# Performance work log

Measured on AMD Instinct MI355X. Metric: run time of the kernel, lower is better.

The kernel has to match this reference:

```python
import jax, jax.numpy as jnp
import numpy as np

GAMMA = 2.0
EPS = 1e-06
LAMBDA_DISTANCE = 1.0
LAMBDA_NORMAL = 0.01
LAMBDA_LAPLACIAN = 0.1
CLS = 1


def vertex_normals(v, f, eps=EPS):
    # v: [N,3], f: [F,3] int. Scatter face normals to vertices, then normalize.
    fv = v[f]  # [F,3,3]
    fn = jnp.cross(fv[:, 1] - fv[:, 0], fv[:, 2] - fv[:, 0])  # [F,3]
    vn = jnp.zeros_like(v)
    vn = vn.at[f[:, 0]].add(fn).at[f[:, 1]].add(fn).at[f[:, 2]].add(fn)
    norm = jnp.maximum(jnp.linalg.norm(vn, axis=-1, keepdims=True), eps)
    return vn / norm


def squared_cdist(a, b):
    # [Na,3] x [Nb,3] -> squared euclidean distances [Na,Nb] (clamped >= 0)
    a2 = jnp.sum(a * a, axis=1)[:, None]
    b2 = jnp.sum(b * b, axis=1)[None, :]
    d2 = a2 + b2 - 2.0 * (a @ b.T)
    return jnp.maximum(d2, 0.0)


def sample_binary_targets(label, v, cls=CLS):
    # Nearest-neighbor grid_sample, align_corners=True, padding zeros.
    # grid = 2*v - 1 -> voxel index = round(v * (size-1)); v[:,0]->W, v[:,1]->H, v[:,2]->D.
    D, H, W = label.shape[2], label.shape[3], label.shape[4]
    ix = jnp.round(v[:, 0] * (W - 1)).astype(jnp.int32)
    iy = jnp.round(v[:, 1] * (H - 1)).astype(jnp.int32)
    iz = jnp.round(v[:, 2] * (D - 1)).astype(jnp.int32)
    inb = (ix >= 0) & (ix < W) & (iy >= 0) & (iy < H) & (iz >= 0) & (iz < D)
    ixc = jnp.clip(ix, 0, W - 1)
    iyc = jnp.clip(iy, 0, H - 1)
    izc = jnp.clip(iz, 0, D - 1)
    vals = (label[0, 0, izc, iyc, ixc] == cls).astype(jnp.float32)
    return jnp.where(inb, vals, 0.0)


def spatial_consistency_loss(rel_pos, targets, gamma=GAMMA, eps=EPS):
    p = jnp.clip(rel_pos, eps, 1.0 - eps)
    pos = targets > 0.5
    pc = jnp.sum(pos).astype(p.dtype)
    tot = jnp.asarray(p.shape[0], p.dtype)
    nc = tot - pc
    alpha = nc / (tot + eps)
    lpos = -alpha * jnp.power(1.0 - p, gamma) * jnp.log(p)
    lneg = -(1.0 - alpha) * jnp.power(p, gamma) * jnp.log(1.0 - p)
    return jnp.sum(jnp.where(pos, lpos, lneg)) / (tot + eps)


def laplacian_uniform(v, f):
    # Uniform mesh Laplacian smoothing: || mean(neighbors) - v ||, averaged.
    i = jnp.concatenate([f[:, 0], f[:, 1], f[:, 2], f[:, 1], f[:, 2], f[:, 0]])
    j = jnp.concatenate([f[:, 1], f[:, 2], f[:, 0], f[:, 0], f[:, 1], f[:, 2]])
    nsum = jnp.zeros_like(v).at[i].add(v[j])
    deg = jnp.zeros((v.shape[0],), v.dtype).at[i].add(1.0)
    lap = nsum / jnp.maximum(deg, 1.0)[:, None] - v
    return jnp.mean(jnp.linalg.norm(lap, axis=1))


def loss_forward(pred_vertices, relative_positions, gt_vertices, pred_faces, gt_faces, label):
    gt_v = jax.lax.stop_gradient(gt_vertices)  # gt comes from label volume; detached in original
    gt_normals = vertex_normals(gt_v, gt_faces)
    # spatial (focal-style) loss
    targets = sample_binary_targets(label, pred_vertices)
    spatial = spatial_consistency_loss(relative_positions, targets)
    # chamfer-style squared surface distance
    d2 = squared_cdist(pred_vertices, gt_v)  # [Np,Ng]
    distance = jnp.mean(jnp.min(d2, axis=1)) + jnp.mean(jnp.min(d2, axis=0))
    # normal consistency vs nearest gt vertex
    pred_normals = vertex_normals(pred_vertices, pred_faces)
    nearest = jnp.argmin(d2, axis=1)
    normal = jnp.mean((pred_normals - gt_normals[nearest]) ** 2)
    # uniform laplacian smoothing
    laplacian = laplacian_uniform(pred_vertices, pred_faces)
    total = spatial + LAMBDA_DISTANCE * distance + LAMBDA_NORMAL * normal + LAMBDA_LAPLACIAN * laplacian
    return total


def setup_inputs() -> dict:
    key = jax.random.key(0)
    k1, k2, k3, k4, k5, k6 = jax.random.split(key, 6)
    Np, Ng = 8192, 12000
    pred_vertices = jax.random.uniform(k1, (Np, 3), dtype=jnp.float32)
    relative_positions = jax.random.uniform(k2, (Np,), dtype=jnp.float32)
    gt_vertices = jax.random.uniform(k3, (Ng, 3), dtype=jnp.float32)
    pred_faces = jax.random.randint(k4, (2 * Np, 3), 0, Np, dtype=jnp.int32)
    gt_faces = jax.random.randint(k5, (2 * Ng, 3), 0, Ng, dtype=jnp.int32)
    label = jax.random.randint(k6, (1, 1, 96, 96, 96), 0, 2, dtype=jnp.int32)
    return {"pred_vertices": pred_vertices, "relative_positions": relative_positions,
            "gt_vertices": gt_vertices, "pred_faces": pred_faces,
            "gt_faces": gt_faces, "label": label}


def reference(pred_vertices, relative_positions, gt_vertices, pred_faces, gt_faces, label):
    return loss_forward(pred_vertices, relative_positions, gt_vertices, pred_faces, gt_faces, label)
```

## Files before the change

### kernel.cpp

```cpp
#include <hip/hip_runtime.h>
#include <math.h>

#define NP 8192
#define NG 12000
#define NFP 16384
#define NFG 24000
#define EPSF 1e-6f

#define GR 16
#define NC (GR*GR*GR)
#define HCELL 0.0625f
#define QL 16

#define N_ZERO 101545
#define ZERO_BLOCKS ((N_ZERO + 1023) / 1024)
#define D1_BLOCKS (2 + ZERO_BLOCKS)

#define QPBLK 64
#define PQB (NP / QPBLK)
#define GQB ((NG + QPBLK - 1) / QPBLK)
#define FB  ((NFG + NFP + 1023) / 1024)
#define D2_BLOCKS (PQB + GQB + FB)

#define CAPP  4608
#define CWCAP 1312

#define FIN_BLOCKS (NP / 256)

static constexpr size_t OFF_STARTP = 0;
static constexpr size_t OFF_STARTG = 16640;
static constexpr size_t OFF_SORTP  = 33280;
static constexpr size_t OFF_SORTG  = 164352;
static constexpr size_t OFF_GTN    = 356352;
static constexpr size_t OFF_PNN    = 500352;
static constexpr size_t OFF_NSUM   = 598656;
static constexpr size_t OFF_DEG    = 696960;
static constexpr size_t OFF_NEAR   = 729728;
static constexpr size_t OFF_ACCUM  = 762496;
static constexpr size_t OFF_DONE   = 762528;

__device__ __forceinline__ int cell_of(float x) {
    int c = (int)(x * (float)GR);
    return min(max(c, 0), GR - 1);
}

__device__ __forceinline__ void build_cells(const float* __restrict__ pts, int n,
                                            unsigned* __restrict__ start,
                                            float4* __restrict__ sorted,
                                            unsigned* h, unsigned* wsum) {
    int t = threadIdx.x;
    int lane = t & 63, wid = t >> 6;
    for (int i = t; i < NC; i += 1024) h[i] = 0u;
    __syncthreads();
    for (int i = t; i < n; i += 1024) {
        int c = (cell_of(pts[3*i+2]) * GR + cell_of(pts[3*i+1])) * GR + cell_of(pts[3*i]);
        atomicAdd(&h[c], 1u);
    }
    __syncthreads();
    unsigned a0 = h[4*t], a1 = h[4*t+1], a2 = h[4*t+2], a3 = h[4*t+3];
    unsigned tsum = a0 + a1 + a2 + a3;
    unsigned x = tsum;
    #pragma unroll
    for (int off = 1; off < 64; off <<= 1) {
        unsigned y = __shfl_up(x, off, 64);
        if (lane >= off) x += y;
    }
    if (lane == 63) wsum[wid] = x;
    __syncthreads();
    if (t < 16) {
        unsigned w = wsum[t];
        #pragma unroll
        for (int off = 1; off < 16; off <<= 1) {
            unsigned y = __shfl_up(w, off, 64);
            if (t >= off) w += y;
        }
        wsum[t] = w;
    }
    __syncthreads();
    unsigned base = (wid ? wsum[wid-1] : 0u) + (x - tsum);
    unsigned e0 = base, e1 = base + a0, e2 = base + a0 + a1, e3 = base + a0 + a1 + a2;
    start[4*t] = e0; start[4*t+1] = e1; start[4*t+2] = e2; start[4*t+3] = e3;
    h[4*t] = e0; h[4*t+1] = e1; h[4*t+2] = e2; h[4*t+3] = e3;
    __syncthreads();
    for (int i = t; i < n; i += 1024) {
        float px = pts[3*i], py = pts[3*i+1], pz = pts[3*i+2];
        int c = (cell_of(pz) * GR + cell_of(py)) * GR + cell_of(px);
        unsigned pos = atomicAdd(&h[c], 1u);
        sorted[pos] = make_float4(px, py, pz, __int_as_float(i));
    }
    if (t == 0) start[NC] = (unsigned)n;
}

__global__ __launch_bounds__(1024) void build_kernel(const float* __restrict__ pred,
                                                     const float* __restrict__ gt,
                                                     unsigned* __restrict__ startP,
                                                     unsigned* __restrict__ startG,
                                                     float4* __restrict__ sortP,
                                                     float4* __restrict__ sortG,
                                                     float* __restrict__ zero) {
    __shared__ unsigned h[NC];
    __shared__ unsigned wsum[16];
    if (blockIdx.x == 0) {
        build_cells(pred, NP, startP, sortP, h, wsum);
    } else if (blockIdx.x == 1) {
        build_cells(gt, NG, startG, sortG, h, wsum);
    } else {
        int i = (blockIdx.x - 2) * 1024 + threadIdx.x;
        if (i < N_ZERO) zero[i] = 0.0f;
    }
}

__device__ __forceinline__ float wave_sum(float x) {
    #pragma unroll
    for (int o = 32; o > 0; o >>= 1) x += __shfl_down(x, o, 64);
    return x;
}

__device__ __forceinline__ unsigned long long u64min(unsigned long long a,
                                                     unsigned long long b) {
    return a < b ? a : b;
}

__device__ __forceinline__ unsigned long long pack_key(float px, float py, float pz,
                                                       float4 q) {
    float ddx = px - q.x, ddy = py - q.y, ddz = pz - q.z;
    float d2 = fmaf(ddx, ddx, fmaf(ddy, ddy, ddz*ddz));
    return ((unsigned long long)__float_as_uint(d2) << 32) |
           (unsigned)__float_as_int(q.w);
}

__device__ unsigned long long group_nn(int lane, float px, float py, float pz,
                                       const float4* __restrict__ Sg,
                                       const unsigned* __restrict__ CSg,
                                       const float4* Sl, const unsigned* CSl,
                                       int c_lo, unsigned p_lo, bool staged) {
    int cx = cell_of(px), cy = cell_of(py), cz = cell_of(pz);
    unsigned long long best = 0xFFFFFFFFFFFFFFFFULL;
    {
        int x0 = max(cx - 1, 0), x1 = min(cx + 1, GR - 1);
        unsigned long long lb = 0xFFFFFFFFFFFFFFFFULL;
        for (int k = lane; k < 9; k += QL) {
            int z = cz + k / 3 - 1, y = cy + k % 3 - 1;
            if (z >= 0 && z < GR && y >= 0 && y < GR) {
                int rowbase = (z * GR + y) * GR;
                if (staged) {
                    unsigned s0 = CSl[rowbase + x0 - c_lo];
                    unsigned s1 = CSl[rowbase + x1 + 1 - c_lo];
                    for (unsigned u = s0; u < s1; ++u)
                        lb = u64min(lb, pack_key(px, py, pz, Sl[u - p_lo]));
                } else {
                    unsigned s0 = CSg[rowbase + x0];
                    unsigned s1 = CSg[rowbase + x1 + 1];
                    for (unsigned u = s0; u < s1; ++u)
                        lb = u64min(lb, pack_key(px, py, pz, Sg[u]));
                }
            }
        }
        best = lb;
        #pragma unroll
        for (int m = 1; m < QL; m <<= 1)
            best = u64min(best, (unsigned long long)__shfl_xor((long long)best, m, 64));
        bool covered = (cx - 1 <= 0) & (cx + 1 >= GR - 1) &
                       (cy - 1 <= 0) & (cy + 1 >= GR - 1) &
                       (cz - 1 <= 0) & (cz + 1 >= GR - 1);
        float blo = 1.0e30f;
        if (cx - 1 > 0)      blo = fminf(blo, px - (float)(cx - 1) * HCELL);
        if (cx + 1 < GR - 1) blo = fminf(blo, (float)(cx + 2) * HCELL - px);
        if (cy - 1 > 0)      blo = fminf(blo, py - (float)(cy - 1) * HCELL);
        if (cy + 1 < GR - 1) blo = fminf(blo, (float)(cy + 2) * HCELL - py);
        if (cz - 1 > 0)      blo = fminf(blo, pz - (float)(cz - 1) * HCELL);
        if (cz + 1 < GR - 1) blo = fminf(blo, (float)(cz + 2) * HCELL - pz);
        float bd2 = __uint_as_float((unsigned)(best >> 32));
        if (covered || (bd2 <= blo * blo)) return best;
    }
    for (int r = 2; ; ++r) {
        int w = 2 * r + 1;
        int nrows = w * w;
        int x0 = max(cx - r, 0), x1 = min(cx + r, GR - 1);
        unsigned long long lb = 0xFFFFFFFFFFFFFFFFULL;
        for (int k = lane; k < nrows; k += QL) {
            int z = cz + k / w - r, y = cy + k % w - r;
            if (z >= 0 && z < GR && y >= 0 && y < GR) {
                int rowbase = (z * GR + y) * GR;
                unsigned s0 = CSg[rowbase + x0];
                unsigned s1 = CSg[rowbase + x1 + 1];
                for (unsigned u = s0; u < s1; ++u)
                    lb = u64min(lb, pack_key(px, py, pz, Sg[u]));
            }
        }
        best = u64min(best, lb);
        #pragma unroll
        for (int m = 1; m < QL; m <<= 1)
            best = u64min(best, (unsigned long long)__shfl_xor((long long)best, m, 64));
        bool covered = (cx - r <= 0) & (cx + r >= GR - 1) &
                       (cy - r <= 0) & (cy + r >= GR - 1) &
                       (cz - r <= 0) & (cz + r >= GR - 1);
        if (covered) break;
        float blo = 1.0e30f;
        if (cx - r > 0)      blo = fminf(blo, px - (float)(cx - r) * HCELL);
        if (cx + r < GR - 1) blo = fminf(blo, (float)(cx + r + 1) * HCELL - px);
        if (cy - r > 0)      blo = fminf(blo, py - (float)(cy - r) * HCELL);
        if (cy + r < GR - 1) blo = fminf(blo, (float)(cy + r + 1) * HCELL - py);
        if (cz - r > 0)      blo = fminf(blo, pz - (float)(cz - r) * HCELL);
        if (cz + r < GR - 1) blo = fminf(blo, (float)(cz + r + 1) * HCELL - pz);
        float bd2 = __uint_as_float((unsigned)(best >> 32));
        if (bd2 <= blo * blo) break;
    }
    return best;
}

__global__ __launch_bounds__(1024) void work_kernel(const float* __restrict__ pred,
                                                    const int* __restrict__ pf,
                                                    const float* __restrict__ gt,
                                                    const int* __restrict__ gf,
                                                    const float4* __restrict__ sortP,
                                                    const float4* __restrict__ sortG,
                                                    const unsigned* __restrict__ startP,
                                                    const unsigned* __restrict__ startG,
                                                    float* __restrict__ gtn,
                                                    float* __restrict__ pnn,
                                                    float* __restrict__ nsum,
                                                    float* __restrict__ deg,
                                                    int* __restrict__ nearestIdx,
                                                    float* __restrict__ accum) {
    __shared__ float4 lpts[CAPP];
    __shared__ unsigned lcs[CWCAP];
    __shared__ float qacc;
    __shared__ int s_info[4];
    int b = blockIdx.x, t = threadIdx.x;

    if (b < PQB + GQB) {
        bool is_pred = (b < PQB);
        const float4*   Q  = is_pred ? sortP  : sortG;
        const float4*   S  = is_pred ? sortG  : sortP;
        const unsigned* CS = is_pred ? startG : startP;
        int qbase = (is_pred ? b : (b - PQB)) * QPBLK;
        int nq = min(QPBLK, (is_pred ? NP : NG) - qbase);

        if (t == 0) {
            qacc = 0.0f;
            float4 qf = Q[qbase], ql = Q[qbase + nq - 1];
            int z_lo = cell_of(qf.z), z_hi = cell_of(ql.z);
            int c_lo  = max(z_lo - 1, 0) * (GR * GR);
            int c_end = min(z_hi + 2, GR) * (GR * GR);
            int cw = c_end - c_lo + 1;
            unsigned p_lo = CS[c_lo], p_hi = CS[c_end];
            int np = (int)(p_hi - p_lo);
            bool ok = (cw <= CWCAP) && (np <= CAPP);
            s_info[0] = c_lo; s_info[1] = (int)p_lo; s_info[2] = np;
            s_info[3] = ok ? cw : -cw;
        }
        __syncthreads();
        int c_lo = s_info[0];
        unsigned p_lo = (unsigned)s_info[1];
        int np = s_info[2];
        int cw = s_info[3];
        bool staged = (cw > 0);
        if (staged) {
            for (int i = t; i < np; i += 1024) lpts[i] = S[p_lo + i];
            for (int i = t; i < cw; i += 1024) lcs[i]  = CS[c_lo + i];
        }
        __syncthreads();

        int lane = t & (QL - 1), group = t >> 4;
        float r0 = 0.0f;
        if (group < nq) {
            int qid = qbase + group;
            float4 P = Q[qid];
            unsigned long long key = group_nn(lane, P.x, P.y, P.z, S, CS,
                                              lpts, lcs, c_lo, p_lo, staged);
            if (lane == 0) {
                r0 = __uint_as_float((unsigned)(key >> 32));
                if (is_pred)
                    nearestIdx[__float_as_int(P.w)] = (int)(unsigned)(key & 0xffffffffu);
            }
        }
        r0 = wave_sum(r0);
        if ((t & 63) == 0) atomicAdd(&qacc, r0);
        __syncthreads();
        if (t == 0) atomicAdd(&accum[is_pred ? 0 : 6], qacc);
    } else {
        int f = (b - PQB - GQB) * 1024 + t;
        if (f < NFG) {
            int i0 = gf[3*f], i1 = gf[3*f+1], i2 = gf[3*f+2];
            float ax = gt[3*i0], ay = gt[3*i0+1], az = gt[3*i0+2];
            float bx = gt[3*i1], by = gt[3*i1+1], bz = gt[3*i1+2];
            float cx = gt[3*i2], cy = gt[3*i2+1], cz = gt[3*i2+2];
            float ux = bx-ax, uy = by-ay, uz = bz-az;
            float wx = cx-ax, wy = cy-ay, wz = cz-az;
            float nx = uy*wz - uz*wy, ny = uz*wx - ux*wz, nz = ux*wy - uy*wx;
            atomicAdd(&gtn[3*i0+0], nx); atomicAdd(&gtn[3*i0+1], ny); atomicAdd(&gtn[3*i0+2], nz);
            atomicAdd(&gtn[3*i1+0], nx); atomicAdd(&gtn[3*i1+1], ny); atomicAdd(&gtn[3*i1+2], nz);
            atomicAdd(&gtn[3*i2+0], nx); atomicAdd(&gtn[3*i2+1], ny); atomicAdd(&gtn[3*i2+2], nz);
        } else if (f < NFG + NFP) {
            int u = f - NFG;
            int i0 = pf[3*u], i1 = pf[3*u+1], i2 = pf[3*u+2];
            float ax = pred[3*i0], ay = pred[3*i0+1], az = pred[3*i0+2];
            float bx = pred[3*i1], by = pred[3*i1+1], bz = pred[3*i1+2];
            float cx = pred[3*i2], cy = pred[3*i2+1], cz = pred[3*i2+2];
            float ux = bx-ax, uy = by-ay, uz = bz-az;
            float wx = cx-ax, wy = cy-ay, wz = cz-az;
            float nx = uy*wz - uz*wy, ny = uz*wx - ux*wz, nz = ux*wy - uy*wx;
            atomicAdd(&pnn[3*i0+0], nx); atomicAdd(&pnn[3*i0+1], ny); atomicAdd(&pnn[3*i0+2], nz);
            atomicAdd(&pnn[3*i1+0], nx); atomicAdd(&pnn[3*i1+1], ny); atomicAdd(&pnn[3*i1+2], nz);
            atomicAdd(&pnn[3*i2+0], nx); atomicAdd(&pnn[3*i2+1], ny); atomicAdd(&pnn[3*i2+2], nz);
            atomicAdd(&nsum[3*i0+0], bx+cx); atomicAdd(&nsum[3*i0+1], by+cy); atomicAdd(&nsum[3*i0+2], bz+cz);
            atomicAdd(&nsum[3*i1+0], cx+ax); atomicAdd(&nsum[3*i1+1], cy+ay); atomicAdd(&nsum[3*i1+2], cz+az);
            atomicAdd(&nsum[3*i2+0], ax+bx); atomicAdd(&nsum[3*i2+1], ay+by); atomicAdd(&nsum[3*i2+2], az+bz);
            atomicAdd(&deg[i0], 2.0f); atomicAdd(&deg[i1], 2.0f); atomicAdd(&deg[i2], 2.0f);
        }
    }
}

__global__ __launch_bounds__(256) void finish_kernel(const float* __restrict__ pred,
                                                     const float* __restrict__ relpos,
                                                     const int* __restrict__ label,
                                                     const float* __restrict__ pnn,
                                                     const float* __restrict__ gtn,
                                                     const float* __restrict__ nsum,
                                                     const float* __restrict__ deg,
                                                     const int* __restrict__ nearestIdx,
                                                     float* __restrict__ accum,
                                                     unsigned* __restrict__ done,
                                                     float* __restrict__ out) {
    int v = blockIdx.x * 256 + threadIdx.x;
    float px = pred[3*v], py = pred[3*v+1], pz = pred[3*v+2];
    int nearest = nearestIdx[v];

    float ax = pnn[3*v], ay = pnn[3*v+1], az = pnn[3*v+2];
    float an = fmaxf(sqrtf(ax*ax + ay*ay + az*az), EPSF);
    float gx = gtn[3*nearest], gy = gtn[3*nearest+1], gz = gtn[3*nearest+2];
    float gn = fmaxf(sqrtf(gx*gx + gy*gy + gz*gz), EPSF);
    float nx = ax/an - gx/gn, ny = ay/an - gy/gn, nz = az/an - gz/gn;
    float sse = nx*nx + ny*ny + nz*nz;

    float d = fmaxf(deg[v], 1.0f);
    float lx = nsum[3*v]/d - px, ly = nsum[3*v+1]/d - py, lz = nsum[3*v+2]/d - pz;
    float lapn = sqrtf(lx*lx + ly*ly + lz*lz);

    int ix = (int)rintf(px * 95.0f), iy = (int)rintf(py * 95.0f), iz = (int)rintf(pz * 95.0f);
    bool inb = (ix >= 0) & (ix < 96) & (iy >= 0) & (iy < 96) & (iz >= 0) & (iz < 96);
    int ixc = min(max(ix, 0), 95), iyc = min(max(iy, 0), 95), izc = min(max(iz, 0), 95);
    bool pos = inb && (label[(izc*96 + iyc)*96 + ixc] == 1);

    float p = fminf(fmaxf(relpos[v], EPSF), 1.0f - EPSF);
    float om = 1.0f - p;
    float pcnt = 0.0f, sx = 0.0f, sy = 0.0f;
    if (pos) { pcnt = 1.0f; sx = om*om*logf(p); }
    else     { sy = p*p*logf(om); }

    float r1 = wave_sum(sse), r2 = wave_sum(lapn), r3 = wave_sum(pcnt);
    float r4 = wave_sum(sx),  r5 = wave_sum(sy);
    __shared__ float bsum[5];
    __shared__ bool isLast;
    if (threadIdx.x < 5) bsum[threadIdx.x] = 0.0f;
    __syncthreads();
    if ((threadIdx.x & 63) == 0) {
        atomicAdd(&bsum[0], r1); atomicAdd(&bsum[1], r2); atomicAdd(&bsum[2], r3);
        atomicAdd(&bsum[3], r4); atomicAdd(&bsum[4], r5);
    }
    __syncthreads();
    if (threadIdx.x == 0) {
        atomicAdd(&accum[1], bsum[0]); atomicAdd(&accum[2], bsum[1]);
        atomicAdd(&accum[3], bsum[2]); atomicAdd(&accum[4], bsum[3]);
        atomicAdd(&accum[5], bsum[4]);
        __threadfence();
        unsigned prev = atomicAdd(done, 1u);
        isLast = (prev == FIN_BLOCKS - 1);
    }
    __syncthreads();
    if (isLast && threadIdx.x == 0) {
        __threadfence();
        float sum_row = __hip_atomic_load(&accum[0], __ATOMIC_RELAXED, __HIP_MEMORY_SCOPE_AGENT);
        float sse_t   = __hip_atomic_load(&accum[1], __ATOMIC_RELAXED, __HIP_MEMORY_SCOPE_AGENT);
        float lap_t   = __hip_atomic_load(&accum[2], __ATOMIC_RELAXED, __HIP_MEMORY_SCOPE_AGENT);
        float pc      = __hip_atomic_load(&accum[3], __ATOMIC_RELAXED, __HIP_MEMORY_SCOPE_AGENT);
        float SX      = __hip_atomic_load(&accum[4], __ATOMIC_RELAXED, __HIP_MEMORY_SCOPE_AGENT);
        float SY      = __hip_atomic_load(&accum[5], __ATOMIC_RELAXED, __HIP_MEMORY_SCOPE_AGENT);
        float sum_col = __hip_atomic_load(&accum[6], __ATOMIC_RELAXED, __HIP_MEMORY_SCOPE_AGENT);
        float tot = (float)NP;
        float alpha = (tot - pc) / (tot + EPSF);
        float spatial = (-alpha * SX - (1.0f - alpha) * SY) / (tot + EPSF);
        float distance = sum_row / (float)NP + sum_col / (float)NG;
        float normal = sse_t / (float)(NP * 3);
        float lapm = lap_t / (float)NP;
        out[0] = spatial + 1.0f * distance + 0.01f * normal + 0.1f * lapm;
    }
}

extern "C" void kernel_launch(void* const* d_in, const int* in_sizes, int n_in,
                              void* d_out, int out_size, void* d_ws, size_t ws_size,
                              hipStream_t stream) {
    const float* pred   = (const float*)d_in[0];
    const float* relpos = (const float*)d_in[1];
    const float* gt     = (const float*)d_in[2];
    const int*   pfaces = (const int*)d_in[3];
    const int*   gfaces = (const int*)d_in[4];
    const int*   label  = (const int*)d_in[5];
    float* out = (float*)d_out;

    char* ws = (char*)d_ws;
    unsigned* startP  = (unsigned*)(ws + OFF_STARTP);
    unsigned* startG  = (unsigned*)(ws + OFF_STARTG);
    float4*   sortP   = (float4*)(ws + OFF_SORTP);
    float4*   sortG   = (float4*)(ws + OFF_SORTG);
    float*    gtn     = (float*)(ws + OFF_GTN);
    float*    pnn     = (float*)(ws + OFF_PNN);
    float*    nsum    = (float*)(ws + OFF_NSUM);
    float*    deg     = (float*)(ws + OFF_DEG);
    int*      nearest = (int*)(ws + OFF_NEAR);
    float*    accum   = (float*)(ws + OFF_ACCUM);
    unsigned* done    = (unsigned*)(ws + OFF_DONE);

    hipLaunchKernelGGL(build_kernel, dim3(D1_BLOCKS), dim3(1024), 0, stream,
                       pred, gt, startP, startG, sortP, sortG,
                       (float*)(ws + OFF_GTN));
    hipLaunchKernelGGL(work_kernel, dim3(D2_BLOCKS), dim3(1024), 0, stream,
                       pred, pfaces, gt, gfaces, sortP, sortG, startP, startG,
                       gtn, pnn, nsum, deg, nearest, accum);
    hipLaunchKernelGGL(finish_kernel, dim3(FIN_BLOCKS), dim3(256), 0, stream,
                       pred, relpos, label, pnn, gtn, nsum, deg, nearest,
                       accum, done, out);
}
```

Baseline: 132.2 us.

## Move face scatter into build kernel, zero with memset, split query kernel

The face-normal and Laplacian scatter atomics move from the query kernel into the build kernel, so they run alongside the two single-block grid builds instead of competing with the NN queries. Workspace zeroing becomes a hipMemsetAsync ahead of the build kernel. The first NN ring now iterates the 27 individual neighbour cells instead of 9 x-rows. The cost is an extra memset launch, and the per-cell loop spreads the work over more lanes but adds more index lookups.

```diff
diff --git a/kernel.cpp b/kernel.cpp
--- a/kernel.cpp
+++ b/kernel.cpp
@@ -12,15 +12,13 @@
 #define HCELL 0.0625f
 #define QL 16
 
-#define N_ZERO 101545
-#define ZERO_BLOCKS ((N_ZERO + 1023) / 1024)
-#define D1_BLOCKS (2 + ZERO_BLOCKS)
+#define FB ((NFG + NFP + 1023) / 1024)
+#define D1_BLOCKS (2 + FB)
 
 #define QPBLK 64
 #define PQB (NP / QPBLK)
 #define GQB ((NG + QPBLK - 1) / QPBLK)
-#define FB  ((NFG + NFP + 1023) / 1024)
-#define D2_BLOCKS (PQB + GQB + FB)
+#define D2_BLOCKS (PQB + GQB)
 
 #define CAPP  4608
 #define CWCAP 1312
@@ -38,6 +36,7 @@
 static constexpr size_t OFF_NEAR   = 729728;
 static constexpr size_t OFF_ACCUM  = 762496;
 static constexpr size_t OFF_DONE   = 762528;
+static constexpr size_t ZERO_BYTES = OFF_DONE + 4 - OFF_GTN;
 
 __device__ __forceinline__ int cell_of(float x) {
     int c = (int)(x * (float)GR);
@@ -91,22 +90,55 @@
     if (t == 0) start[NC] = (unsigned)n;
 }
 
-__global__ __launch_bounds__(1024) void build_kernel(const float* __restrict__ pred,
-                                                     const float* __restrict__ gt,
-                                                     unsigned* __restrict__ startP,
-                                                     unsigned* __restrict__ startG,
-                                                     float4* __restrict__ sortP,
-                                                     float4* __restrict__ sortG,
-                                                     float* __restrict__ zero) {
+__global__ __launch_bounds__(1024) void build_face_kernel(const float* __restrict__ pred,
+                                                          const float* __restrict__ gt,
+                                                          const int* __restrict__ pf,
+                                                          const int* __restrict__ gf,
+                                                          unsigned* __restrict__ startP,
+                                                          unsigned* __restrict__ startG,
+                                                          float4* __restrict__ sortP,
+                                                          float4* __restrict__ sortG,
+                                                          float* __restrict__ gtn,
+                                                          float* __restrict__ pnn,
+                                                          float* __restrict__ nsum,
+                                                          float* __restrict__ deg) {
     __shared__ unsigned h[NC];
     __shared__ unsigned wsum[16];
-    if (blockIdx.x == 0) {
+    int b = blockIdx.x, t = threadIdx.x;
+    if (b == 0) {
         build_cells(pred, NP, startP, sortP, h, wsum);
-    } else if (blockIdx.x == 1) {
+    } else if (b == 1) {
         build_cells(gt, NG, startG, sortG, h, wsum);
     } else {
-        int i = (blockIdx.x - 2) * 1024 + threadIdx.x;
-        if (i < N_ZERO) zero[i] = 0.0f;
+        int f = (b - 2) * 1024 + t;
+        if (f < NFG) {
+            int i0 = gf[3*f], i1 = gf[3*f+1], i2 = gf[3*f+2];
+            float ax = gt[3*i0], ay = gt[3*i0+1], az = gt[3*i0+2];
+            float bx = gt[3*i1], by = gt[3*i1+1], bz = gt[3*i1+2];
+            float cx = gt[3*i2], cy = gt[3*i2+1], cz = gt[3*i2+2];
+            float ux = bx-ax, uy = by-ay, uz = bz-az;
+            float wx = cx-ax, wy = cy-ay, wz = cz-az;
+            float nx = uy*wz - uz*wy, ny = uz*wx - ux*wz, nz = ux*wy - uy*wx;
+            atomicAdd(&gtn[3*i0+0], nx); atomicAdd(&gtn[3*i0+1], ny); atomicAdd(&gtn[3*i0+2], nz);
+            atomicAdd(&gtn[3*i1+0], nx); atomicAdd(&gtn[3*i1+1], ny); atomicAdd(&gtn[3*i1+2], nz);
+            atomicAdd(&gtn[3*i2+0], nx); atomicAdd(&gtn[3*i2+1], ny); atomicAdd(&gtn[3*i2+2], nz);
+        } else if (f < NFG + NFP) {
+            int u = f - NFG;
+            int i0 = pf[3*u], i1 = pf[3*u+1], i2 = pf[3*u+2];
+            float ax = pred[3*i0], ay = pred[3*i0+1], az = pred[3*i0+2];
+            float bx = pred[3*i1], by = pred[3*i1+1], bz = pred[3*i1+2];
+            float cx = pred[3*i2], cy = pred[3*i2+1], cz = pred[3*i2+2];
+            float ux = bx-ax, uy = by-ay, uz = bz-az;
+            float wx = cx-ax, wy = cy-ay, wz = cz-az;
+            float nx = uy*wz - uz*wy, ny = uz*wx - ux*wz, nz = ux*wy - uy*wx;
+            atomicAdd(&pnn[3*i0+0], nx); atomicAdd(&pnn[3*i0+1], ny); atomicAdd(&pnn[3*i0+2], nz);
+            atomicAdd(&pnn[3*i1+0], nx); atomicAdd(&pnn[3*i1+1], ny); atomicAdd(&pnn[3*i1+2], nz);
+            atomicAdd(&pnn[3*i2+0], nx); atomicAdd(&pnn[3*i2+1], ny); atomicAdd(&pnn[3*i2+2], nz);
+            atomicAdd(&nsum[3*i0+0], bx+cx); atomicAdd(&nsum[3*i0+1], by+cy); atomicAdd(&nsum[3*i0+2], bz+cz);
+            atomicAdd(&nsum[3*i1+0], cx+ax); atomicAdd(&nsum[3*i1+1], cy+ay); atomicAdd(&nsum[3*i1+2], cz+az);
+            atomicAdd(&nsum[3*i2+0], ax+bx); atomicAdd(&nsum[3*i2+1], ay+by); atomicAdd(&nsum[3*i2+2], az+bz);
+            atomicAdd(&deg[i0], 2.0f); atomicAdd(&deg[i1], 2.0f); atomicAdd(&deg[i2], 2.0f);
+        }
     }
 }
 
@@ -137,20 +169,19 @@
     int cx = cell_of(px), cy = cell_of(py), cz = cell_of(pz);
     unsigned long long best = 0xFFFFFFFFFFFFFFFFULL;
     {
-        int x0 = max(cx - 1, 0), x1 = min(cx + 1, GR - 1);
         unsigned long long lb = 0xFFFFFFFFFFFFFFFFULL;
-        for (int k = lane; k < 9; k += QL) {
-            int z = cz + k / 3 - 1, y = cy + k % 3 - 1;
-            if (z >= 0 && z < GR && y >= 0 && y < GR) {
-                int rowbase = (z * GR + y) * GR;
+        for (int k = lane; k < 27; k += QL) {
+            int z = cz + k / 9 - 1, y = cy + (k % 9) / 3 - 1, x = cx + k % 3 - 1;
+            if (((unsigned)z < GR) & ((unsigned)y < GR) & ((unsigned)x < GR)) {
+                int c = (z * GR + y) * GR + x;
                 if (staged) {
-                    unsigned s0 = CSl[rowbase + x0 - c_lo];
-                    unsigned s1 = CSl[rowbase + x1 + 1 - c_lo];
+                    unsigned s0 = CSl[c - c_lo];
+                    unsigned s1 = CSl[c + 1 - c_lo];
                     for (unsigned u = s0; u < s1; ++u)
                         lb = u64min(lb, pack_key(px, py, pz, Sl[u - p_lo]));
                 } else {
-                    unsigned s0 = CSg[rowbase + x0];
-                    unsigned s1 = CSg[rowbase + x1 + 1];
+                    unsigned s0 = CSg[c];
+                    unsigned s1 = CSg[c + 1];
                     for (unsigned u = s0; u < s1; ++u)
                         lb = u64min(lb, pack_key(px, py, pz, Sg[u]));
                 }
@@ -209,107 +240,67 @@
     return best;
 }
 
-__global__ __launch_bounds__(1024) void work_kernel(const float* __restrict__ pred,
-                                                    const int* __restrict__ pf,
-                                                    const float* __restrict__ gt,
-                                                    const int* __restrict__ gf,
-                                                    const float4* __restrict__ sortP,
-                                                    const float4* __restrict__ sortG,
-                                                    const unsigned* __restrict__ startP,
-                                                    const unsigned* __restrict__ startG,
-                                                    float* __restrict__ gtn,
-                                                    float* __restrict__ pnn,
-                                                    float* __restrict__ nsum,
-                                                    float* __restrict__ deg,
-                                                    int* __restrict__ nearestIdx,
-                                                    float* __restrict__ accum) {
+__global__ __launch_bounds__(1024) void query_kernel(const float4* __restrict__ sortP,
+                                                     const float4* __restrict__ sortG,
+                                                     const unsigned* __restrict__ startP,
+                                                     const unsigned* __restrict__ startG,
+                                                     int* __restrict__ nearestIdx,
+                                                     float* __restrict__ accum) {
     __shared__ float4 lpts[CAPP];
     __shared__ unsigned lcs[CWCAP];
     __shared__ float qacc;
     __shared__ int s_info[4];
     int b = blockIdx.x, t = threadIdx.x;
 
-    if (b < PQB + GQB) {
-        bool is_pred = (b < PQB);
-        const float4*   Q  = is_pred ? sortP  : sortG;
-        const float4*   S  = is_pred ? sortG  : sortP;
-        const unsigned* CS = is_pred ? startG : startP;
-        int qbase = (is_pred ? b : (b - PQB)) * QPBLK;
-        int nq = min(QPBLK, (is_pred ? NP : NG) - qbase);
-
-        if (t == 0) {
-            qacc = 0.0f;
-            float4 qf = Q[qbase], ql = Q[qbase + nq - 1];
-            int z_lo = cell_of(qf.z), z_hi = cell_of(ql.z);
-            int c_lo  = max(z_lo - 1, 0) * (GR * GR);
-            int c_end = min(z_hi + 2, GR) * (GR * GR);
-            int cw = c_end - c_lo + 1;
-            unsigned p_lo = CS[c_lo], p_hi = CS[c_end];
-            int np = (int)(p_hi - p_lo);
-            bool ok = (cw <= CWCAP) && (np <= CAPP);
-            s_info[0] = c_lo; s_info[1] = (int)p_lo; s_info[2] = np;
-            s_info[3] = ok ? cw : -cw;
+    bool is_pred = (b < PQB);
+    const float4*   Q  = is_pred ? sortP  : sortG;
+    const float4*   S  = is_pred ? sortG  : sortP;
+    const unsigned* CS = is_pred ? startG : startP;
+    int qbase = (is_pred ? b : (b - PQB)) * QPBLK;
+    int nq = min(QPBLK, (is_pred ? NP : NG) - qbase);
+
+    if (t == 0) {
+        qacc = 0.0f;
+        float4 qf = Q[qbase], ql = Q[qbase + nq - 1];
+        int z_lo = cell_of(qf.z), z_hi = cell_of(ql.z);
+        int c_lo  = max(z_lo - 1, 0) * (GR * GR);
+        int c_end = min(z_hi + 2, GR) * (GR * GR);
+        int cw = c_end - c_lo + 1;
+        unsigned p_lo = CS[c_lo], p_hi = CS[c_end];
+        int np = (int)(p_hi - p_lo);
+        bool ok = (cw <= CWCAP) && (np <= CAPP);
+        s_info[0] = c_lo; s_info[1] = (int)p_lo; s_info[2] = np;
+        s_info[3] = ok ? cw : -cw;
+    }
+    __syncthreads();
+    int c_lo = s_info[0];
+    unsigned p_lo = (unsigned)s_info[1];
+    int np = s_info[2];
+    int cw = s_info[3];
+    bool staged = (cw > 0);
+    if (staged) {
+        for (int i = t; i < np; i += 1024) lpts[i] = S[p_lo + i];
+        for (int i = t; i < cw; i += 1024) lcs[i]  = CS[c_lo + i];
+    }
+    __syncthreads();
+
+    int lane = t & (QL - 1), group = t >> 4;
+    float r0 = 0.0f;
+    if (group < nq) {
+        int qid = qbase + group;
+        float4 P = Q[qid];
+        unsigned long long key = group_nn(lane, P.x, P.y, P.z, S, CS,
+                                          lpts, lcs, c_lo, p_lo, staged);
+        if (lane == 0) {
+            r0 = __uint_as_float((unsigned)(key >> 32));
+            if (is_pred)
+                nearestIdx[__float_as_int(P.w)] = (int)(unsigned)(key & 0xffffffffu);
         }
-        __syncthreads();
-        int c_lo = s_info[0];
-        unsigned p_lo = (unsigned)s_info[1];
-        int np = s_info[2];
-        int cw = s_info[3];
-        bool staged = (cw > 0);
-        if (staged) {
-            for (int i = t; i < np; i += 1024) lpts[i] = S[p_lo + i];
-            for (int i = t; i < cw; i += 1024) lcs[i]  = CS[c_lo + i];
-        }
-        __syncthreads();
-
-        int lane = t & (QL - 1), group = t >> 4;
-        float r0 = 0.0f;
-        if (group < nq) {
-            int qid = qbase + group;
-            float4 P = Q[qid];
-            unsigned long long key = group_nn(lane, P.x, P.y, P.z, S, CS,
-                                              lpts, lcs, c_lo, p_lo, staged);
-            if (lane == 0) {
-                r0 = __uint_as_float((unsigned)(key >> 32));
-                if (is_pred)
-                    nearestIdx[__float_as_int(P.w)] = (int)(unsigned)(key & 0xffffffffu);
-            }
-        }
-        r0 = wave_sum(r0);
-        if ((t & 63) == 0) atomicAdd(&qacc, r0);
-        __syncthreads();
-        if (t == 0) atomicAdd(&accum[is_pred ? 0 : 6], qacc);
-    } else {
-        int f = (b - PQB - GQB) * 1024 + t;
-        if (f < NFG) {
-            int i0 = gf[3*f], i1 = gf[3*f+1], i2 = gf[3*f+2];
-            float ax = gt[3*i0], ay = gt[3*i0+1], az = gt[3*i0+2];
-            float bx = gt[3*i1], by = gt[3*i1+1], bz = gt[3*i1+2];
-            float cx = gt[3*i2], cy = gt[3*i2+1], cz = gt[3*i2+2];
-            float ux = bx-ax, uy = by-ay, uz = bz-az;
-            float wx = cx-ax, wy = cy-ay, wz = cz-az;
-            float nx = uy*wz - uz*wy, ny = uz*wx - ux*wz, nz = ux*wy - uy*wx;
-            atomicAdd(&gtn[3*i0+0], nx); atomicAdd(&gtn[3*i0+1], ny); atomicAdd(&gtn[3*i0+2], nz);
-            atomicAdd(&gtn[3*i1+0], nx); atomicAdd(&gtn[3*i1+1], ny); atomicAdd(&gtn[3*i1+2], nz);
-            atomicAdd(&gtn[3*i2+0], nx); atomicAdd(&gtn[3*i2+1], ny); atomicAdd(&gtn[3*i2+2], nz);
-        } else if (f < NFG + NFP) {
-            int u = f - NFG;
-            int i0 = pf[3*u], i1 = pf[3*u+1], i2 = pf[3*u+2];
-            float ax = pred[3*i0], ay = pred[3*i0+1], az = pred[3*i0+2];
-            float bx = pred[3*i1], by = pred[3*i1+1], bz = pred[3*i1+2];
-            float cx = pred[3*i2], cy = pred[3*i2+1], cz = pred[3*i2+2];
-            float ux = bx-ax, uy = by-ay, uz = bz-az;
-            float wx = cx-ax, wy = cy-ay, wz = cz-az;
-            float nx = uy*wz - uz*wy, ny = uz*wx - ux*wz, nz = ux*wy - uy*wx;
-            atomicAdd(&pnn[3*i0+0], nx); atomicAdd(&pnn[3*i0+1], ny); atomicAdd(&pnn[3*i0+2], nz);
-            atomicAdd(&pnn[3*i1+0], nx); atomicAdd(&pnn[3*i1+1], ny); atomicAdd(&pnn[3*i1+2], nz);
-            atomicAdd(&pnn[3*i2+0], nx); atomicAdd(&pnn[3*i2+1], ny); atomicAdd(&pnn[3*i2+2], nz);
-            atomicAdd(&nsum[3*i0+0], bx+cx); atomicAdd(&nsum[3*i0+1], by+cy); atomicAdd(&nsum[3*i0+2], bz+cz);
-            atomicAdd(&nsum[3*i1+0], cx+ax); atomicAdd(&nsum[3*i1+1], cy+ay); atomicAdd(&nsum[3*i1+2], cz+az);
-            atomicAdd(&nsum[3*i2+0], ax+bx); atomicAdd(&nsum[3*i2+1], ay+by); atomicAdd(&nsum[3*i2+2], az+bz);
-            atomicAdd(&deg[i0], 2.0f); atomicAdd(&deg[i1], 2.0f); atomicAdd(&deg[i2], 2.0f);
-        }
-    }
+    }
+    r0 = wave_sum(r0);
+    if ((t & 63) == 0) atomicAdd(&qacc, r0);
+    __syncthreads();
+    if (t == 0) atomicAdd(&accum[is_pred ? 0 : 6], qacc);
 }
 
 __global__ __launch_bounds__(256) void finish_kernel(const float* __restrict__ pred,
@@ -412,12 +403,12 @@
     float*    accum   = (float*)(ws + OFF_ACCUM);
     unsigned* done    = (unsigned*)(ws + OFF_DONE);
 
-    hipLaunchKernelGGL(build_kernel, dim3(D1_BLOCKS), dim3(1024), 0, stream,
-                       pred, gt, startP, startG, sortP, sortG,
-                       (float*)(ws + OFF_GTN));
-    hipLaunchKernelGGL(work_kernel, dim3(D2_BLOCKS), dim3(1024), 0, stream,
-                       pred, pfaces, gt, gfaces, sortP, sortG, startP, startG,
-                       gtn, pnn, nsum, deg, nearest, accum);
+    hipMemsetAsync(ws + OFF_GTN, 0, ZERO_BYTES, stream);
+    hipLaunchKernelGGL(build_face_kernel, dim3(D1_BLOCKS), dim3(1024), 0, stream,
+                       pred, gt, pfaces, gfaces, startP, startG, sortP, sortG,
+                       gtn, pnn, nsum, deg);
+    hipLaunchKernelGGL(query_kernel, dim3(D2_BLOCKS), dim3(1024), 0, stream,
+                       sortP, sortG, startP, startG, nearest, accum);
     hipLaunchKernelGGL(finish_kernel, dim3(FIN_BLOCKS), dim3(256), 0, stream,
                        pred, relpos, label, pnn, gtn, nsum, deg, nearest,
                        accum, done, out);
```

New measurement: 131.2 us. About the same (-0.8%).
